# Optimization experiments

Hardware: AMD Instinct MI355X
Metric: run time of the kernel (lower is better)

## Reference

```python
import jax, jax.numpy as jnp
import numpy as np

K = 16            # top-k negatives kept per row
TEMP = 0.01       # softmax temperature
V = 0.95          # geometric decay base
NEG_FILL = -1e9   # masks out same-class entries before topk (never selected since k << #negatives)


def _l2norm(x):
    # torch F.normalize: x / max(||x||, eps)
    n = jnp.linalg.norm(x, axis=-1, keepdims=True)
    return x / jnp.maximum(n, 1e-12)


def setup_inputs() -> dict:
    key = jax.random.key(0)
    k1, k2, k3 = jax.random.split(key, 3)
    feature = jax.random.normal(k1, (4096, 128), dtype=jnp.float32)
    negative_features = jax.random.normal(k2, (4, 4096, 128), dtype=jnp.float32)
    target = jax.random.randint(k3, (4096,), 0, 4)
    return {"feature": feature, "target": target,
            "negative_features": negative_features, "idx": 0}


def reference(feature, target, negative_features, idx):
    J = negative_features.shape[0]
    f = _l2norm(feature)                       # [n, d]
    negs = _l2norm(negative_features)          # [J, n, d]
    # cosine similarity for every negative set: [J, n, n]
    sims = jnp.einsum('nd,jmd->jnm', f, negs)
    # same-class mask, applied only to the idx-th set
    same = target[:, None] == target[None, :]  # [n, n]
    sims = sims.at[idx].set(jnp.where(same, NEG_FILL, sims[idx]))
    # per-row top-k over the last (candidate) dim: [J, n, K]
    top, _ = jax.lax.top_k(sims, K)
    logits = jnp.transpose(top, (1, 0, 2)) / TEMP   # [n, J, K]
    p = jax.nn.softmax(logits, axis=1)
    logp = jax.nn.log_softmax(logits, axis=1)
    ent = jnp.sum(p * logp, axis=1)                 # [n, K]
    decay = V ** jnp.arange(K, dtype=jnp.float32)
    decay = decay / jnp.sum(decay)                  # L1-normalized, matches F.normalize(p=1)
    loss = jnp.mean(jnp.sum(ent * decay, axis=1)) + jnp.log(jnp.float32(J))
    return loss
```

## Files before the change

### kernel.cpp

```cpp
#include <hip/hip_runtime.h>
#include <hip/hip_bf16.h>
#include <math.h>

#define N 4096
#define D 128
#define NJ 4
#define KTOP 16
#define CSPLIT 2

typedef __attribute__((ext_vector_type(8))) short bf16x8;
typedef __attribute__((ext_vector_type(4))) float f32x4;


__device__ __forceinline__ void ce_desc(float* a, int i, int l) {
    float x = a[i], y = a[l];
    a[i] = fmaxf(x, y);
    a[l] = fminf(x, y);
}

__device__ __forceinline__ void sort16_desc(float* a) {
    ce_desc(a,0,1);  ce_desc(a,2,3);  ce_desc(a,0,2);  ce_desc(a,1,3);  ce_desc(a,1,2);
    ce_desc(a,4,5);  ce_desc(a,6,7);  ce_desc(a,4,6);  ce_desc(a,5,7);  ce_desc(a,5,6);
    ce_desc(a,0,4);  ce_desc(a,2,6);  ce_desc(a,2,4);  ce_desc(a,1,5);  ce_desc(a,3,7);
    ce_desc(a,3,5);  ce_desc(a,1,2);  ce_desc(a,3,4);  ce_desc(a,5,6);
    ce_desc(a,8,9);  ce_desc(a,10,11); ce_desc(a,8,10); ce_desc(a,9,11); ce_desc(a,9,10);
    ce_desc(a,12,13); ce_desc(a,14,15); ce_desc(a,12,14); ce_desc(a,13,15); ce_desc(a,13,14);
    ce_desc(a,8,12); ce_desc(a,10,14); ce_desc(a,10,12); ce_desc(a,9,13); ce_desc(a,11,15);
    ce_desc(a,11,13); ce_desc(a,9,10); ce_desc(a,11,12); ce_desc(a,13,14);
    ce_desc(a,0,8);  ce_desc(a,4,12); ce_desc(a,4,8);  ce_desc(a,2,10); ce_desc(a,6,14);
    ce_desc(a,6,10); ce_desc(a,2,4);  ce_desc(a,6,8);  ce_desc(a,10,12);
    ce_desc(a,1,9);  ce_desc(a,5,13); ce_desc(a,5,9);  ce_desc(a,3,11); ce_desc(a,7,15);
    ce_desc(a,7,11); ce_desc(a,3,5);  ce_desc(a,7,9);  ce_desc(a,11,13);
    ce_desc(a,1,2);  ce_desc(a,3,4);  ce_desc(a,5,6);  ce_desc(a,7,8);  ce_desc(a,9,10);
    ce_desc(a,11,12); ce_desc(a,13,14);
}

__device__ __forceinline__ void bitonic_clean16_desc(float* a) {
    #pragma unroll
    for (int jj = 8; jj > 0; jj >>= 1) {
        #pragma unroll
        for (int i = 0; i < 16; i++) {
            int l = i ^ jj;
            if (l > i) {
                float x = a[i], y = a[l];
                a[i] = fmaxf(x, y);
                a[l] = fminf(x, y);
            }
        }
    }
}

__global__ __launch_bounds__(256) void neguni_prep(
    const float* __restrict__ feat, const float* __restrict__ negs,
    unsigned short* __restrict__ fh, unsigned short* __restrict__ gh,
    float* __restrict__ out)
{
    __shared__ unsigned short lbuf[8192];

    if (blockIdx.x == 0 && threadIdx.x == 0) *out = 0.f;

    if (blockIdx.x < 256) {
        const int w    = threadIdx.x >> 6;
        const int lane = threadIdx.x & 63;
        const int p    = lane & 15;
        const int rr   = lane >> 4;
        const int row  = blockIdx.x * 16 + w * 4 + rr;

        const float* src = feat + (size_t)row * D;
        float4 v0 = ((const float4*)src)[p * 2];
        float4 v1 = ((const float4*)src)[p * 2 + 1];
        float ss = v0.x*v0.x + v0.y*v0.y + v0.z*v0.z + v0.w*v0.w
                 + v1.x*v1.x + v1.y*v1.y + v1.z*v1.z + v1.w*v1.w;
        ss += __shfl_xor(ss, 1, 64);
        ss += __shfl_xor(ss, 2, 64);
        ss += __shfl_xor(ss, 4, 64);
        ss += __shfl_xor(ss, 8, 64);
        const float inv = 1.0f / fmaxf(sqrtf(ss), 1e-12f);

        float f[8] = {v0.x, v0.y, v0.z, v0.w, v1.x, v1.y, v1.z, v1.w};
        unsigned int u[4];
        #pragma unroll
        for (int i = 0; i < 4; i++) {
            __hip_bfloat16 b0 = __float2bfloat16(f[2*i]   * inv);
            __hip_bfloat16 b1 = __float2bfloat16(f[2*i+1] * inv);
            u[i] = ((unsigned int)*(unsigned short*)&b1 << 16) | *(unsigned short*)&b0;
        }
        uint4 pk; pk.x = u[0]; pk.y = u[1]; pk.z = u[2]; pk.w = u[3];
        *(uint4*)(fh + (size_t)row * D + p * 8) = pk;
    } else {
        const int c   = blockIdx.x - 256;
        const int j   = c >> 6;
        const int chg = c & 63;
        const int t   = threadIdx.x;
        const int lr  = t >> 2;
        const int p4  = t & 3;

        const float* src = negs + ((size_t)(j * 4096 + chg * 64 + lr)) * D + p4 * 32;
        float4 v[8];
        float ss = 0.f;
        #pragma unroll
        for (int i = 0; i < 8; i++) {
            v[i] = ((const float4*)src)[i];
            ss += v[i].x*v[i].x + v[i].y*v[i].y + v[i].z*v[i].z + v[i].w*v[i].w;
        }
        ss += __shfl_xor(ss, 1, 64);
        ss += __shfl_xor(ss, 2, 64);
        const float inv = 1.0f / fmaxf(sqrtf(ss), 1e-12f);

        float f[32];
        #pragma unroll
        for (int i = 0; i < 8; i++) {
            f[4*i]   = v[i].x; f[4*i+1] = v[i].y;
            f[4*i+2] = v[i].z; f[4*i+3] = v[i].w;
        }

        const int t16 = lr >> 4;
        const int col = lr & 15;
        #pragma unroll
        for (int qq = 0; qq < 4; qq++) {
            unsigned int uu[4];
            #pragma unroll
            for (int h = 0; h < 4; h++) {
                __hip_bfloat16 b0 = __float2bfloat16(f[qq*8 + 2*h]     * inv);
                __hip_bfloat16 b1 = __float2bfloat16(f[qq*8 + 2*h + 1] * inv);
                uu[h] = ((unsigned int)*(unsigned short*)&b1 << 16) | *(unsigned short*)&b0;
            }
            uint4 pk; pk.x = uu[0]; pk.y = uu[1]; pk.z = uu[2]; pk.w = uu[3];
            *(uint4*)(lbuf + (p4 * 4 + t16) * 512 + (qq * 16 + col) * 8) = pk;
        }
        __syncthreads();

        uint4* dst = (uint4*)(gh + (size_t)j * N * D + (size_t)chg * 8192);
        const uint4* sb = (const uint4*)lbuf;
        dst[t]       = sb[t];
        dst[t + 256] = sb[t + 256];
        dst[t + 512] = sb[t + 512];
        dst[t + 768] = sb[t + 768];
    }
}

__global__ __launch_bounds__(256, 4) void neguni_main(
    const unsigned short* __restrict__ fh, const unsigned short* __restrict__ gh,
    const int* __restrict__ target, const int* __restrict__ idxp,
    float* __restrict__ topbuf)
{
    __shared__ float tops[4][16][17];

    const int tid   = threadIdx.x;
    const int w     = tid >> 6;
    const int lane  = tid & 63;
    const int col16 = lane & 15;
    const int quad  = lane >> 4;

    const int j   = blockIdx.x & 3;
    const int ft  = (blockIdx.x >> 2) & 255;
    const int cs  = blockIdx.x >> 10;
    const int r0  = ft * 16;
    const int c0  = cs * 2048 + w * 512;
    const int idx = idxp[0];
    const bool msk = (j == idx);

    bf16x8 bfr[4];
    {
        const unsigned short* fr = fh + (size_t)(r0 + col16) * D + quad * 8;
        bfr[0] = *(const bf16x8*)(fr);
        bfr[1] = *(const bf16x8*)(fr + 32);
        bfr[2] = *(const bf16x8*)(fr + 64);
        bfr[3] = *(const bf16x8*)(fr + 96);
    }
    const int rtg = target[r0 + col16];

    float lst[KTOP];

    const int chg0 = cs * 32 + w * 8;
    const unsigned short* ab0 = gh + (size_t)j * N * D + (size_t)chg0 * 8192 + lane * 8;

    #pragma unroll 1
    for (int ch = 0; ch < 8; ch++) {
        const unsigned short* ab = ab0 + (size_t)ch * 8192;

        f32x4 acc[4];
        #pragma unroll
        for (int t = 0; t < 4; t++) acc[t] = (f32x4){0.f, 0.f, 0.f, 0.f};

        #pragma unroll
        for (int s = 0; s < 4; s++) {
            #pragma unroll
            for (int t = 0; t < 4; t++) {
                bf16x8 a = *(const bf16x8*)(ab + (s * 4 + t) * 512);
                acc[t] = __builtin_amdgcn_mfma_f32_16x16x32_bf16(a, bfr[s], acc[t], 0, 0, 0);
            }
        }

        const int cbase = c0 + ch * 64;
        float s16[16];
        #pragma unroll
        for (int t = 0; t < 4; t++) {
            s16[t * 4 + 0] = acc[t][0];
            s16[t * 4 + 1] = acc[t][1];
            s16[t * 4 + 2] = acc[t][2];
            s16[t * 4 + 3] = acc[t][3];
        }
        if (msk) {
            #pragma unroll
            for (int t = 0; t < 4; t++) {
                int4 tc = *(const int4*)(target + cbase + t * 16 + quad * 4);
                if (tc.x == rtg) s16[t * 4 + 0] = -1e9f;
                if (tc.y == rtg) s16[t * 4 + 1] = -1e9f;
                if (tc.z == rtg) s16[t * 4 + 2] = -1e9f;
                if (tc.w == rtg) s16[t * 4 + 3] = -1e9f;
            }
        }

        sort16_desc(s16);
        if (ch == 0) {
            #pragma unroll
            for (int i = 0; i < 16; i++) lst[i] = s16[i];
        } else {
            float mg[16];
            #pragma unroll
            for (int i = 0; i < 16; i++) mg[i] = fmaxf(lst[i], s16[15 - i]);
            bitonic_clean16_desc(mg);
            #pragma unroll
            for (int i = 0; i < 16; i++) lst[i] = mg[i];
        }
    }

    #pragma unroll
    for (int off = 16; off <= 32; off <<= 1) {
        float mg[16];
        #pragma unroll
        for (int i = 0; i < 16; i++)
            mg[i] = fmaxf(lst[i], __shfl_xor(lst[15 - i], off, 64));
        bitonic_clean16_desc(mg);
        #pragma unroll
        for (int i = 0; i < 16; i++) lst[i] = mg[i];
    }

    if (lane < 16) {
        #pragma unroll
        for (int i = 0; i < 16; i++) tops[w][lane][i] = lst[i];
        tops[w][lane][16] = -3.0e38f;
    }
    __syncthreads();

    if (tid < 16) {
        int i0 = 0, i1 = 0, i2 = 0, i3 = 0;
        float* outp = topbuf + (((size_t)j * N + r0 + tid) * CSPLIT + cs) * KTOP;
        #pragma unroll
        for (int k = 0; k < KTOP; k++) {
            float v0 = tops[0][tid][i0], v1 = tops[1][tid][i1];
            float v2 = tops[2][tid][i2], v3 = tops[3][tid][i3];
            float m01 = fmaxf(v0, v1), m23 = fmaxf(v2, v3);
            float mx  = fmaxf(m01, m23);
            if      (mx == v0) i0++;
            else if (mx == v1) i1++;
            else if (mx == v2) i2++;
            else               i3++;
            outp[k] = mx;
        }
    }
}

__global__ __launch_bounds__(64) void neguni_fin(
    const float* __restrict__ topbuf, float* __restrict__ out)
{
    __shared__ float buf[64][35];
    __shared__ float mm[16][65];

    const int t     = threadIdx.x;
    const int j     = t >> 4;
    const int row_l = t & 15;
    const int row   = blockIdx.x * 16 + row_l;

    const float4* src = (const float4*)(topbuf + ((size_t)j * N + row) * (CSPLIT * KTOP));
    #pragma unroll
    for (int q = 0; q < 8; q++) {
        float4 v = src[q];
        const int base = (q >> 2) * 17 + (q & 3) * 4;
        buf[t][base + 0] = v.x;
        buf[t][base + 1] = v.y;
        buf[t][base + 2] = v.z;
        buf[t][base + 3] = v.w;
    }
    buf[t][16] = -3.0e38f;
    buf[t][33] = -3.0e38f;

    {
        int ia = 0, ib = 17;
        #pragma unroll
        for (int k = 0; k < KTOP; k++) {
            float va = buf[t][ia], vb = buf[t][ib];
            bool ta = va >= vb;
            mm[row_l][k * 4 + j] = ta ? va : vb;
            if (ta) ia++; else ib++;
        }
    }
    __syncthreads();

    float val = 0.f;
    #pragma unroll
    for (int i = 0; i < 4; i++) {
        const int idx2 = t + i * 64;
        const int rl   = idx2 & 15;
        const int k    = idx2 >> 4;
        float l0 = mm[rl][k * 4 + 0] * 100.0f;
        float l1 = mm[rl][k * 4 + 1] * 100.0f;
        float l2 = mm[rl][k * 4 + 2] * 100.0f;
        float l3 = mm[rl][k * 4 + 3] * 100.0f;
        float m  = fmaxf(fmaxf(l0, l1), fmaxf(l2, l3));
        float d0 = l0 - m, d1 = l1 - m, d2 = l2 - m, d3 = l3 - m;
        float e0 = __expf(d0), e1 = __expf(d1), e2 = __expf(d2), e3 = __expf(d3);
        float s  = e0 + e1 + e2 + e3;
        float ent = (e0 * d0 + e1 * d1 + e2 * d2 + e3 * d3) / s - __logf(s);
        float dk  = __expf(-0.05129329439f * (float)k);
        val += ent * dk;
    }
    val *= (1.0f / (11.1974666f * (float)N));

    #pragma unroll
    for (int off = 32; off > 0; off >>= 1) val += __shfl_xor(val, off, 64);
    if (t == 0) {
        atomicAdd(out, val);
        if (blockIdx.x == 0) atomicAdd(out, 1.38629436112f);
    }
}

extern "C" void kernel_launch(void* const* d_in, const int* in_sizes, int n_in,
                              void* d_out, int out_size, void* d_ws, size_t ws_size,
                              hipStream_t stream) {
    const float* feat   = (const float*)d_in[0];
    const int*   target = (const int*)d_in[1];
    const float* negs   = (const float*)d_in[2];
    const int*   idxp   = (const int*)d_in[3];
    float* out = (float*)d_out;

    unsigned short* fh = (unsigned short*)d_ws;
    unsigned short* gh = fh + (size_t)N * D;
    float* topbuf      = (float*)(gh + (size_t)NJ * N * D);

    neguni_prep<<<dim3(512), dim3(256), 0, stream>>>(feat, negs, fh, gh, out);
    neguni_main<<<dim3(NJ * (N / 16) * CSPLIT), dim3(256), 0, stream>>>(fh, gh, target, idxp, topbuf);
    neguni_fin<<<dim3(N / 16), dim3(64), 0, stream>>>(topbuf, out);
}
```

Baseline: 134.2 us.

## Share negative chunks across waves via double-buffered LDS async loads

Each block now covers 64 feature rows, one 16-row slice per wave, and all four waves scan the same 2048 candidate columns. Candidate tiles are staged into LDS with global_load_lds in a double-buffered loop, so each negative tile is fetched from global memory once per block instead of once per wave. The cross-wave LDS merge of top-k lists is dropped because each wave now owns whole rows and writes its list directly. The cost is a block-wide barrier every chunk, a longer serial loop per wave, a quarter as many blocks, and launch bounds relaxed to two blocks per CU.

```diff
diff --git a/kernel.cpp b/kernel.cpp
--- a/kernel.cpp
+++ b/kernel.cpp
@@ -139,12 +139,12 @@
     }
 }
 
-__global__ __launch_bounds__(256, 4) void neguni_main(
+__global__ __launch_bounds__(256, 2) void neguni_main(
     const unsigned short* __restrict__ fh, const unsigned short* __restrict__ gh,
     const int* __restrict__ target, const int* __restrict__ idxp,
     float* __restrict__ topbuf)
 {
-    __shared__ float tops[4][16][17];
+    __shared__ unsigned short lbuf[2][8192];
 
     const int tid   = threadIdx.x;
     const int w     = tid >> 6;
@@ -153,41 +153,65 @@
     const int quad  = lane >> 4;
 
     const int j   = blockIdx.x & 3;
-    const int ft  = (blockIdx.x >> 2) & 255;
-    const int cs  = blockIdx.x >> 10;
-    const int r0  = ft * 16;
-    const int c0  = cs * 2048 + w * 512;
+    const int ft  = (blockIdx.x >> 2) & 63;
+    const int cs  = blockIdx.x >> 8;
+    const int r0  = ft * 64;
+    const int row = r0 + w * 16 + col16;
+    const int c0  = cs * 2048;
     const int idx = idxp[0];
     const bool msk = (j == idx);
 
     bf16x8 bfr[4];
     {
-        const unsigned short* fr = fh + (size_t)(r0 + col16) * D + quad * 8;
+        const unsigned short* fr = fh + (size_t)row * D + quad * 8;
         bfr[0] = *(const bf16x8*)(fr);
         bfr[1] = *(const bf16x8*)(fr + 32);
         bfr[2] = *(const bf16x8*)(fr + 64);
         bfr[3] = *(const bf16x8*)(fr + 96);
     }
-    const int rtg = target[r0 + col16];
+    const int rtg = target[row];
+
+    const unsigned short* gcs = gh + (size_t)j * N * D + (size_t)cs * 32 * 8192;
 
     float lst[KTOP];
 
-    const int chg0 = cs * 32 + w * 8;
-    const unsigned short* ab0 = gh + (size_t)j * N * D + (size_t)chg0 * 8192 + lane * 8;
+    {
+        const unsigned short* gsrc = gcs + w * 2048 + lane * 8;
+        unsigned short* ldst = &lbuf[0][w * 2048];
+        #pragma unroll
+        for (int i = 0; i < 4; i++) {
+            __builtin_amdgcn_global_load_lds(
+                (const __attribute__((address_space(1))) void*)(gsrc + i * 512),
+                (__attribute__((address_space(3))) void*)(ldst + i * 512),
+                16, 0, 0);
+        }
+    }
 
     #pragma unroll 1
-    for (int ch = 0; ch < 8; ch++) {
-        const unsigned short* ab = ab0 + (size_t)ch * 8192;
-
+    for (int ch = 0; ch < 32; ch++) {
+        __syncthreads();
+
+        if (ch < 31) {
+            const unsigned short* gsrc = gcs + (size_t)(ch + 1) * 8192 + w * 2048 + lane * 8;
+            unsigned short* ldst = &lbuf[(ch + 1) & 1][w * 2048];
+            #pragma unroll
+            for (int i = 0; i < 4; i++) {
+                __builtin_amdgcn_global_load_lds(
+                    (const __attribute__((address_space(1))) void*)(gsrc + i * 512),
+                    (__attribute__((address_space(3))) void*)(ldst + i * 512),
+                    16, 0, 0);
+            }
+        }
+
+        const unsigned short* lb = &lbuf[ch & 1][0];
         f32x4 acc[4];
         #pragma unroll
         for (int t = 0; t < 4; t++) acc[t] = (f32x4){0.f, 0.f, 0.f, 0.f};
-
         #pragma unroll
         for (int s = 0; s < 4; s++) {
             #pragma unroll
             for (int t = 0; t < 4; t++) {
-                bf16x8 a = *(const bf16x8*)(ab + (s * 4 + t) * 512);
+                bf16x8 a = *(const bf16x8*)(lb + (s * 4 + t) * 512 + lane * 8);
                 acc[t] = __builtin_amdgcn_mfma_f32_16x16x32_bf16(a, bfr[s], acc[t], 0, 0, 0);
             }
         }
@@ -217,12 +241,9 @@
             #pragma unroll
             for (int i = 0; i < 16; i++) lst[i] = s16[i];
         } else {
-            float mg[16];
-            #pragma unroll
-            for (int i = 0; i < 16; i++) mg[i] = fmaxf(lst[i], s16[15 - i]);
-            bitonic_clean16_desc(mg);
-            #pragma unroll
-            for (int i = 0; i < 16; i++) lst[i] = mg[i];
+            #pragma unroll
+            for (int i = 0; i < 16; i++) lst[i] = fmaxf(lst[i], s16[15 - i]);
+            bitonic_clean16_desc(lst);
         }
     }
 
@@ -237,28 +258,10 @@
         for (int i = 0; i < 16; i++) lst[i] = mg[i];
     }
 
-    if (lane < 16) {
-        #pragma unroll
-        for (int i = 0; i < 16; i++) tops[w][lane][i] = lst[i];
-        tops[w][lane][16] = -3.0e38f;
-    }
-    __syncthreads();
-
-    if (tid < 16) {
-        int i0 = 0, i1 = 0, i2 = 0, i3 = 0;
-        float* outp = topbuf + (((size_t)j * N + r0 + tid) * CSPLIT + cs) * KTOP;
-        #pragma unroll
-        for (int k = 0; k < KTOP; k++) {
-            float v0 = tops[0][tid][i0], v1 = tops[1][tid][i1];
-            float v2 = tops[2][tid][i2], v3 = tops[3][tid][i3];
-            float m01 = fmaxf(v0, v1), m23 = fmaxf(v2, v3);
-            float mx  = fmaxf(m01, m23);
-            if      (mx == v0) i0++;
-            else if (mx == v1) i1++;
-            else if (mx == v2) i2++;
-            else               i3++;
-            outp[k] = mx;
-        }
+    if (quad == 0) {
+        float* outp = topbuf + (((size_t)j * N + r0 + w * 16 + col16) * CSPLIT + cs) * KTOP;
+        #pragma unroll
+        for (int k = 0; k < KTOP; k++) outp[k] = lst[k];
     }
 }
 
@@ -340,6 +343,6 @@
     float* topbuf      = (float*)(gh + (size_t)NJ * N * D);
 
     neguni_prep<<<dim3(512), dim3(256), 0, stream>>>(feat, negs, fh, gh, out);
-    neguni_main<<<dim3(NJ * (N / 16) * CSPLIT), dim3(256), 0, stream>>>(fh, gh, target, idxp, topbuf);
+    neguni_main<<<dim3(NJ * (N / 64) * CSPLIT), dim3(256), 0, stream>>>(fh, gh, target, idxp, topbuf);
     neguni_fin<<<dim3(N / 16), dim3(64), 0, stream>>>(topbuf, out);
 }
```

Measured after the change: 133.1 us. About the same (-0.8%).
